# Performance work log

Hardware: AMD Instinct MI355X
Metric: run time of the kernel (lower is better)

The kernel has to match this reference:

```python
import jax, jax.numpy as jnp
import numpy as np

B, T, C, E = 16, 1024, 256, 512
NUM_CENTER = [512, 256, 128]
NUM_NNS = [16, 32, 64]
BN_EPS = 1e-5


def _fps(pts, K):
    # farthest point sampling, deterministic start at index 0. pts: [B,N,3] -> [B,K] int32
    N = pts.shape[1]
    def one(p):
        def step(carry, _):
            d, cur = carry
            dist = jnp.sum((p - p[cur]) ** 2, axis=-1)
            d = jnp.minimum(d, dist)
            nxt = jnp.argmax(d).astype(jnp.int32)
            return (d, nxt), cur
        init = (jnp.full((N,), jnp.inf, p.dtype), jnp.int32(0))
        _, idxs = jax.lax.scan(step, init, None, length=K)
        return idxs
    return jax.vmap(one)(pts)


def _knn(q, t, k):
    # k nearest neighbors of each query q [B,Tq,3] among targets t [B,Tt,3] -> [B,Tq,k]
    d2 = (jnp.sum(q * q, -1)[:, :, None] + jnp.sum(t * t, -1)[:, None, :]
          - 2.0 * jnp.einsum('bqc,btc->bqt', q, t))
    _, idx = jax.lax.top_k(-d2, k)
    return idx


def _gather(x, idx):
    # x [B,N,C], idx [B,M] -> [B,M,C]
    return jax.vmap(lambda xb, ib: xb[ib])(x, idx)


def _knn_gather(x, idx):
    # x [B,N,C], idx [B,M,K] -> [B,M,K,C]
    return jax.vmap(lambda xb, ib: xb[ib])(x, idx)


def _bn(x, g, b):
    # training-mode BatchNorm1d over leading (batch) dim of [N,C]
    m = jnp.mean(x, axis=0)
    v = jnp.mean((x - m) ** 2, axis=0)
    return (x - m) * jax.lax.rsqrt(v + BN_EPS) * g + b


def reference(tokens, centers, lrfs, wq, wkv, mlp_w1, mlp_b1, mlp_w2, mlp_b2,
              bn1_g, bn1_b, bn2_g, bn2_b, att_w1, att_b1, att_w2, att_b2,
              emb_w, emb_b, embn_g, embn_b):
    Bq, Tt, Cd = tokens.shape
    centers_target = centers
    lrfs_target = lrfs.reshape(Bq, Tt, 9)
    tokens_target = tokens
    T_target = Tt
    for i in range(len(NUM_CENTER)):
        Tq = NUM_CENTER[i]
        k = NUM_NNS[i]
        rep_idx = _fps(centers_target, Tq)                      # [B,Tq]
        centers_query = _gather(centers_target, rep_idx)        # [B,Tq,3]
        lrfs_query = _gather(lrfs_target, rep_idx)              # [B,Tq,9]
        tokens_query = _gather(tokens_target, rep_idx)          # [B,Tq,C]
        nn_idx = _knn(centers_query, centers_target, k)         # [B,Tq,k]
        skip = tokens_query.reshape(Bq * Tq, Cd)
        if i > 0:
            t = jnp.concatenate([tokens_query, tokens_target], axis=1)
            t = _bn(t.reshape(Bq * (Tq + T_target), Cd), bn1_g[i], bn1_b[i])
            t = t.reshape(Bq, Tq + T_target, Cd)
            tokens_query, tokens_target = t[:, :Tq, :], t[:, Tq:, :]
        Q = tokens_query @ wq[i]                                # [B,Tq,C]
        KV = tokens_target @ wkv[i]                             # [B,Tt,2C]
        Kf, Vf = KV[..., :Cd], KV[..., Cd:]
        Kn = _knn_gather(Kf, nn_idx).reshape(Bq * Tq, k, Cd)
        Vn = _knn_gather(Vf, nn_idx).reshape(Bq * Tq, k, Cd)
        Qf = Q.reshape(Bq * Tq, Cd)
        # vector self-attention: elementwise Q-K diff -> MLP -> softmax over neighbors
        diff = Qf[:, None, :] - Kn                              # [B*Tq,k,C]
        sim = jax.nn.relu(diff @ att_w1[i] + att_b1[i]) @ att_w2[i] + att_b2[i]
        A = jax.nn.softmax(sim, axis=1)
        tq = jnp.sum(A * Vn, axis=1)                            # [B*Tq,C]
        tq = tq + skip
        skip2 = tq
        tq = _bn(tq, bn2_g[i], bn2_b[i])
        tq = jax.nn.relu(tq @ mlp_w1[i] + mlp_b1[i]) @ mlp_w2[i] + mlp_b2[i]
        tq = tq + skip2
        T_target = Tq
        centers_target = centers_query
        lrfs_target = lrfs_query
        tokens_target = tq.reshape(Bq, Tq, Cd)
    g = jnp.mean(tokens_target, axis=1)                         # [B,C]
    g = jax.nn.relu(_bn(g @ emb_w + emb_b, embn_g, embn_b))     # [B,E]
    # ksparse: keep top-64 activations per row
    vals, _ = jax.lax.top_k(g, 64)
    thr = vals[:, -1:]
    g = jnp.where(g >= thr, g, 0.0)
    n = jnp.maximum(jnp.linalg.norm(g, axis=1, keepdims=True), 1e-12)
    return g / n


def setup_inputs() -> dict:
    key = jax.random.key(0)
    ks = jax.random.split(key, 10)
    s = 0.05
    return {
        'tokens': jax.random.normal(ks[0], (B, T, C), jnp.float32),
        'centers': jax.random.normal(ks[1], (B, T, 3), jnp.float32),
        'lrfs': jax.random.normal(ks[2], (B, T, 3, 3), jnp.float32),
        'wq': jax.random.normal(ks[3], (3, C, C), jnp.float32) * s,
        'wkv': jax.random.normal(ks[4], (3, C, 2 * C), jnp.float32) * s,
        'mlp_w1': jax.random.normal(ks[5], (3, C, 2 * C), jnp.float32) * s,
        'mlp_b1': jnp.zeros((3, 2 * C), jnp.float32),
        'mlp_w2': jax.random.normal(ks[6], (3, 2 * C, C), jnp.float32) * s,
        'mlp_b2': jnp.zeros((3, C), jnp.float32),
        'bn1_g': jnp.ones((3, C), jnp.float32),
        'bn1_b': jnp.zeros((3, C), jnp.float32),
        'bn2_g': jnp.ones((3, C), jnp.float32),
        'bn2_b': jnp.zeros((3, C), jnp.float32),
        'att_w1': jax.random.normal(ks[7], (3, C, C), jnp.float32) * s,
        'att_b1': jnp.zeros((3, C), jnp.float32),
        'att_w2': jax.random.normal(ks[8], (3, C, C), jnp.float32) * s,
        'att_b2': jnp.zeros((3, C), jnp.float32),
        'emb_w': jax.random.normal(ks[9], (C, E), jnp.float32) * s,
        'emb_b': jnp.zeros((E,), jnp.float32),
        'embn_g': jnp.ones((E,), jnp.float32),
        'embn_b': jnp.zeros((E,), jnp.float32),
    }
```

## Files before the change

### kernel.cpp

```cpp
#include <hip/hip_runtime.h>
#include <cstdint>
#include <cmath>

static constexpr int BB = 16;
static constexpr int TT0 = 1024;
static constexpr int CC = 256;
static constexpr int EE = 512;

typedef __bf16 bf16x8 __attribute__((ext_vector_type(8)));
typedef float  f32x4  __attribute__((ext_vector_type(4)));

template <int NPL>
__device__ void fps_body(float4* sp, const float* __restrict__ ctr,
                         int Tt, int Ksel, int* __restrict__ rep,
                         int b, int lane)
{
  const float* base = ctr + (size_t)b * Tt * 3;
  float x[NPL], y[NPL], z[NPL], d[NPL];
  #pragma unroll
  for (int j = 0; j < NPL; ++j) {
    int idx = lane * NPL + j;
    x[j] = base[idx * 3 + 0];
    y[j] = base[idx * 3 + 1];
    z[j] = base[idx * 3 + 2];
    d[j] = INFINITY;
    sp[idx] = make_float4(x[j], y[j], z[j], 0.f);
  }
  int cur = 0;
  for (int s = 0; s < Ksel; ++s) {
    if (lane == 0) rep[b * Ksel + s] = cur;
    float4 cpt = sp[cur];
    unsigned long long key = 0ull;
    #pragma unroll
    for (int j = 0; j < NPL; ++j) {
      float dx = __fsub_rn(x[j], cpt.x);
      float dy = __fsub_rn(y[j], cpt.y);
      float dz = __fsub_rn(z[j], cpt.z);
      float dist = __fadd_rn(__fadd_rn(__fmul_rn(dx, dx), __fmul_rn(dy, dy)),
                             __fmul_rn(dz, dz));
      float nd = fminf(d[j], dist);
      d[j] = nd;
      unsigned long long kj =
          ((unsigned long long)__float_as_uint(nd) << 32) |
          (unsigned)(0xFFFFFFFFu - (unsigned)(lane * NPL + j));
      key = (kj > key) ? kj : key;
    }
    float ld = __uint_as_float((unsigned)(key >> 32));
    float rm = ld;
    {
      int t;
      t = __builtin_amdgcn_mov_dpp(__float_as_int(rm), 0x121, 0xf, 0xf, false);
      rm = fmaxf(rm, __int_as_float(t));
      t = __builtin_amdgcn_mov_dpp(__float_as_int(rm), 0x122, 0xf, 0xf, false);
      rm = fmaxf(rm, __int_as_float(t));
      t = __builtin_amdgcn_mov_dpp(__float_as_int(rm), 0x124, 0xf, 0xf, false);
      rm = fmaxf(rm, __int_as_float(t));
      t = __builtin_amdgcn_mov_dpp(__float_as_int(rm), 0x128, 0xf, 0xf, false);
      rm = fmaxf(rm, __int_as_float(t));
    }
    float r0 = __uint_as_float((unsigned)__builtin_amdgcn_readlane(__float_as_int(rm), 0));
    float r1 = __uint_as_float((unsigned)__builtin_amdgcn_readlane(__float_as_int(rm), 16));
    float r2 = __uint_as_float((unsigned)__builtin_amdgcn_readlane(__float_as_int(rm), 32));
    float r3 = __uint_as_float((unsigned)__builtin_amdgcn_readlane(__float_as_int(rm), 48));
    float gm = fmaxf(fmaxf(r0, r1), fmaxf(r2, r3));
    unsigned long long mask = __ballot(ld == gm);
    int wl = __ffsll(mask) - 1;
    unsigned lowkey = (unsigned)__builtin_amdgcn_readlane((int)(unsigned)key, wl);
    cur = (int)(0xFFFFFFFFu - lowkey);
  }
}

__global__ __launch_bounds__(256) void knn_kernel(
    const float* __restrict__ cq, const float* __restrict__ ct,
    int Tq, int Tt, int Kn, int* __restrict__ nn)
{
  int r = blockIdx.x;
  int b = r / Tq;
  __shared__ float d2[1024];
  __shared__ float wv[4];
  __shared__ int wi[4];
  int tid = threadIdx.x, lane = tid & 63, wid = tid >> 6;
  float qx = cq[(size_t)r * 3 + 0];
  float qy = cq[(size_t)r * 3 + 1];
  float qz = cq[(size_t)r * 3 + 2];
  float sq = __fadd_rn(__fadd_rn(__fmul_rn(qx, qx), __fmul_rn(qy, qy)),
                       __fmul_rn(qz, qz));
  for (int t = tid; t < Tt; t += 256) {
    const float* tp = ct + ((size_t)b * Tt + t) * 3;
    float tx = tp[0], ty = tp[1], tz = tp[2];
    float st = __fadd_rn(__fadd_rn(__fmul_rn(tx, tx), __fmul_rn(ty, ty)),
                         __fmul_rn(tz, tz));
    float dot = __fadd_rn(__fadd_rn(__fmul_rn(qx, tx), __fmul_rn(qy, ty)),
                          __fmul_rn(qz, tz));
    d2[t] = __fsub_rn(__fadd_rn(sq, st), __fmul_rn(2.0f, dot));
  }
  __syncthreads();
  for (int j = 0; j < Kn; ++j) {
    float v = INFINITY; int ix = 0x7fffffff;
    for (int t = tid; t < Tt; t += 256) {
      float dv = d2[t];
      if (dv < v) { v = dv; ix = t; }
    }
    #pragma unroll
    for (int off = 32; off > 0; off >>= 1) {
      float ov = __shfl_down(v, off);
      int oi = __shfl_down(ix, off);
      if (ov < v || (ov == v && oi < ix)) { v = ov; ix = oi; }
    }
    if (lane == 0) { wv[wid] = v; wi[wid] = ix; }
    __syncthreads();
    if (tid == 0) {
      float bv = wv[0]; int bi = wi[0];
      for (int w = 1; w < 4; ++w)
        if (wv[w] < bv || (wv[w] == bv && wi[w] < bi)) { bv = wv[w]; bi = wi[w]; }
      nn[(size_t)r * Kn + j] = bi;
      d2[bi] = INFINITY;
    }
    __syncthreads();
  }
}

__global__ void gather_rows_kernel(
    const float* __restrict__ src, const int* __restrict__ idx,
    float* __restrict__ dst, int Tq, int Tt, int D, int total)
{
  int i = blockIdx.x * blockDim.x + threadIdx.x;
  if (i >= total) return;
  int d = i % D;
  int q = (i / D) % Tq;
  int b = i / (D * Tq);
  int s = idx[b * Tq + q];
  dst[i] = src[((size_t)b * Tt + s) * D + d];
}

__global__ __launch_bounds__(256) void bn_stats_kernel(
    const float* __restrict__ x1, int R1, const float* __restrict__ x2, int R2,
    float* __restrict__ part, int nch)
{
  int c = threadIdx.x;
  int chunk = blockIdx.x;
  int R = R1 + R2;
  int per = (R + nch - 1) / nch;
  int r0 = chunk * per;
  int r1 = min(r0 + per, R);
  float s = 0.f, ss = 0.f;
  for (int r = r0; r < r1; ++r) {
    float v = (r < R1) ? x1[(size_t)r * 256 + c] : x2[(size_t)(r - R1) * 256 + c];
    s += v;
    ss = fmaf(v, v, ss);
  }
  part[(size_t)chunk * 512 + c] = s;
  part[(size_t)chunk * 512 + 256 + c] = ss;
}

__global__ __launch_bounds__(256) void bn_finalize_kernel(
    const float* __restrict__ part, int nch, int R,
    float* __restrict__ mean, float* __restrict__ rstd)
{
  int c = threadIdx.x;
  float s = 0.f, ss = 0.f;
  for (int k = 0; k < nch; ++k) {
    s += part[(size_t)k * 512 + c];
    ss += part[(size_t)k * 512 + 256 + c];
  }
  float m = s / (float)R;
  float v = ss / (float)R - m * m;
  if (v < 0.f) v = 0.f;
  mean[c] = m;
  rstd[c] = rsqrtf(v + 1e-5f);
}

__global__ __launch_bounds__(256) void gemm_kernel(
    const float* __restrict__ A, int lda,
    const float* __restrict__ W, int ldw,
    const float* __restrict__ bias, const float* __restrict__ resid,
    float* __restrict__ out, int M, int N, int K, int relu)
{
  __shared__ float As[32][68];
  __shared__ float Bs[32][68];
  int bm = blockIdx.y * 64;
  int bn = blockIdx.x * 64;
  int tid = threadIdx.x;
  int tx = tid & 15, ty = tid >> 4;
  int arow = tid >> 3;
  int ak = (tid & 7) * 4;
  int wk = tid >> 4;
  int wn = (tid & 15) * 4;
  float acc[4][4] = {{0.f}};
  for (int k0 = 0; k0 < K; k0 += 32) {
    #pragma unroll
    for (int h = 0; h < 2; ++h) {
      int row = bm + arow + h * 32;
      float4 a = (row < M)
          ? *(const float4*)&A[(size_t)row * lda + k0 + ak]
          : make_float4(0.f, 0.f, 0.f, 0.f);
      As[ak + 0][arow + h * 32] = a.x;
      As[ak + 1][arow + h * 32] = a.y;
      As[ak + 2][arow + h * 32] = a.z;
      As[ak + 3][arow + h * 32] = a.w;
    }
    #pragma unroll
    for (int h = 0; h < 2; ++h) {
      int krow = k0 + wk + h * 16;
      *(float4*)&Bs[wk + h * 16][wn] =
          *(const float4*)&W[(size_t)krow * ldw + bn + wn];
    }
    __syncthreads();
    #pragma unroll
    for (int k = 0; k < 32; ++k) {
      float4 a = *(const float4*)&As[k][ty * 4];
      float4 b = *(const float4*)&Bs[k][tx * 4];
      float av[4] = {a.x, a.y, a.z, a.w};
      float bv[4] = {b.x, b.y, b.z, b.w};
      #pragma unroll
      for (int i = 0; i < 4; ++i)
        #pragma unroll
        for (int j = 0; j < 4; ++j)
          acc[i][j] = fmaf(av[i], bv[j], acc[i][j]);
    }
    __syncthreads();
  }
  #pragma unroll
  for (int i = 0; i < 4; ++i) {
    int m = bm + ty * 4 + i;
    if (m >= M) continue;
    #pragma unroll
    for (int j = 0; j < 4; ++j) {
      int n = bn + tx * 4 + j;
      float v = acc[i][j];
      if (bias) v += bias[n];
      if (relu) v = fmaxf(v, 0.f);
      if (resid) v += resid[(size_t)m * N + n];
      out[(size_t)m * N + n] = v;
    }
  }
}

__global__ void splitT_kernel(
    const float* __restrict__ src, int ldw, int K, int N,
    __bf16* __restrict__ hi, __bf16* __restrict__ lo, int total)
{
  int i = blockIdx.x * blockDim.x + threadIdx.x;
  if (i >= total) return;
  int n = i / K;
  int k = i - n * K;
  float v = src[(size_t)k * ldw + n];
  __bf16 h = (__bf16)v;
  hi[i] = h;
  lo[i] = (__bf16)(v - (float)h);
}

__global__ __launch_bounds__(256) void split_w2_kernel(
    const float* __restrict__ w2, __bf16* __restrict__ hi,
    __bf16* __restrict__ lo)
{
  int i = blockIdx.x * 256 + threadIdx.x;
  int s = i >> 16;
  int e = i & 65535;
  int cp = e >> 8;
  int cc = e & 255;
  float v = w2[((size_t)s << 16) + cc * 256 + cp];
  __bf16 h = (__bf16)v;
  hi[i] = h;
  lo[i] = (__bf16)(v - (float)h);
}

template <int NPL>
__global__ __launch_bounds__(256) void gemm_mfma_kernel(
    const float* __restrict__ A, int lda,
    const __bf16* __restrict__ WThi, const __bf16* __restrict__ WTlo,
    const float* __restrict__ bias, const float* __restrict__ resid,
    float* __restrict__ out, int M, int N, int K, int relu,
    const float* __restrict__ bnm, const float* __restrict__ bnr,
    const float* __restrict__ bng, const float* __restrict__ bnb,
    int nbx,
    const float* __restrict__ fps_ctr, int fps_Tt, int fps_Ksel,
    int* __restrict__ fps_rep)
{
  __shared__ __align__(16) float As[128 * 36];
  if ((int)blockIdx.x >= nbx) {
    if (fps_rep == nullptr || (int)blockIdx.y >= BB) return;
    if ((int)threadIdx.x >= 64) return;
    fps_body<NPL>((float4*)As, fps_ctr, fps_Tt, fps_Ksel, fps_rep,
                  blockIdx.y, threadIdx.x);
    return;
  }
  int bm = blockIdx.y * 128;
  int bn = blockIdx.x * 64;
  int tid = threadIdx.x;
  int w = tid >> 6, lane = tid & 63;
  int jl = lane & 15;
  int kg = lane >> 4;

  f32x4 acc[2][4];
  #pragma unroll
  for (int mt = 0; mt < 2; ++mt)
    #pragma unroll
    for (int nt = 0; nt < 4; ++nt) acc[mt][nt] = (f32x4){0.f, 0.f, 0.f, 0.f};

  for (int k0 = 0; k0 < K; k0 += 32) {
    #pragma unroll
    for (int f = 0; f < 4; ++f) {
      int fi = tid + f * 256;
      int row = fi >> 3, c4 = fi & 7;
      float4 v = *(const float4*)&A[(size_t)(bm + row) * lda + k0 + c4 * 4];
      if (bnm) {
        int kk = k0 + c4 * 4;
        float4 m4 = *(const float4*)&bnm[kk];
        float4 r4 = *(const float4*)&bnr[kk];
        float4 g4 = *(const float4*)&bng[kk];
        float4 b4 = *(const float4*)&bnb[kk];
        v.x = (v.x - m4.x) * r4.x * g4.x + b4.x;
        v.y = (v.y - m4.y) * r4.y * g4.y + b4.y;
        v.z = (v.z - m4.z) * r4.z * g4.z + b4.z;
        v.w = (v.w - m4.w) * r4.w * g4.w + b4.w;
      }
      *(float4*)&As[row * 36 + c4 * 4] = v;
    }
    __syncthreads();
    bf16x8 ahi[2], alo[2];
    #pragma unroll
    for (int mt = 0; mt < 2; ++mt) {
      int row = (w * 2 + mt) * 16 + jl;
      float4 a0 = *(const float4*)&As[row * 36 + kg * 8];
      float4 a1 = *(const float4*)&As[row * 36 + kg * 8 + 4];
      float hv[8] = {a0.x, a0.y, a0.z, a0.w, a1.x, a1.y, a1.z, a1.w};
      #pragma unroll
      for (int i = 0; i < 8; ++i) {
        __bf16 t0 = (__bf16)hv[i];
        ahi[mt][i] = t0;
        alo[mt][i] = (__bf16)(hv[i] - (float)t0);
      }
    }
    #pragma unroll
    for (int nt = 0; nt < 4; ++nt) {
      size_t boff = (size_t)(bn + nt * 16 + jl) * K + k0 + kg * 8;
      bf16x8 bhi = *(const bf16x8*)(WThi + boff);
      bf16x8 blo = *(const bf16x8*)(WTlo + boff);
      #pragma unroll
      for (int mt = 0; mt < 2; ++mt) {
        acc[mt][nt] = __builtin_amdgcn_mfma_f32_16x16x32_bf16(alo[mt], bhi, acc[mt][nt], 0, 0, 0);
        acc[mt][nt] = __builtin_amdgcn_mfma_f32_16x16x32_bf16(ahi[mt], blo, acc[mt][nt], 0, 0, 0);
        acc[mt][nt] = __builtin_amdgcn_mfma_f32_16x16x32_bf16(ahi[mt], bhi, acc[mt][nt], 0, 0, 0);
      }
    }
    __syncthreads();
  }
  #pragma unroll
  for (int mt = 0; mt < 2; ++mt)
    #pragma unroll
    for (int nt = 0; nt < 4; ++nt)
      #pragma unroll
      for (int qi = 0; qi < 4; ++qi) {
        int m = bm + (w * 2 + mt) * 16 + kg * 4 + qi;
        int n = bn + nt * 16 + jl;
        float v = acc[mt][nt][qi];
        if (bias) v += bias[n];
        if (relu) v = fmaxf(v, 0.f);
        if (resid) v += resid[(size_t)m * N + n];
        out[(size_t)m * N + n] = v;
      }
}

template <int KN>
__global__ __launch_bounds__(256, 2) void attn5_kernel(
    const float* __restrict__ Qw, const float* __restrict__ KV,
    const int* __restrict__ nn,
    const float* __restrict__ b1, const __bf16* __restrict__ w2Thi,
    const __bf16* __restrict__ w2Tlo, const float* __restrict__ b2,
    const float* __restrict__ skip, float* __restrict__ out, int Tq, int Tt)
{
  constexpr int G  = 128 / KN;
  constexpr int GC = 64 / KN;
  constexpr int LD = 260;
  __shared__ float sim[64 * LD];
  __shared__ int nns[128];
  int r0 = blockIdx.x * G;
  int b = r0 / Tq;
  int tid = threadIdx.x;
  if (tid < 128) nns[tid] = nn[(size_t)r0 * KN + tid];
  __syncthreads();

  int w = tid >> 6, lane = tid & 63;
  int jl = lane & 15;
  int kg = lane >> 4;
  int nt0 = w * 4;
  const float* kvb = KV + (size_t)b * Tt * 512;

  f32x4 acc[8][4];
  #pragma unroll
  for (int m = 0; m < 8; ++m)
    #pragma unroll
    for (int n = 0; n < 4; ++n) acc[m][n] = (f32x4){0.f, 0.f, 0.f, 0.f};

  const float* qp[8];
  const float* kp[8];
  #pragma unroll
  for (int mt = 0; mt < 8; ++mt) {
    int jr = mt * 16 + jl;
    qp[mt] = Qw + (size_t)(r0 + jr / KN) * 256;
    kp[mt] = kvb + (size_t)nns[jr] * 512;
  }

  #pragma unroll
  for (int ks = 0; ks < 8; ++ks) {
    int c0 = ks * 32 + kg * 8;
    float4 b1a = *(const float4*)(b1 + c0);
    float4 b1b = *(const float4*)(b1 + c0 + 4);
    bf16x8 ahi[8], alo[8];
    #pragma unroll
    for (int mt = 0; mt < 8; ++mt) {
      float4 qa = *(const float4*)(qp[mt] + c0);
      float4 qb = *(const float4*)(qp[mt] + c0 + 4);
      float4 ka = *(const float4*)(kp[mt] + c0);
      float4 kb = *(const float4*)(kp[mt] + c0 + 4);
      float h[8];
      h[0] = fmaxf(qa.x - ka.x + b1a.x, 0.f);
      h[1] = fmaxf(qa.y - ka.y + b1a.y, 0.f);
      h[2] = fmaxf(qa.z - ka.z + b1a.z, 0.f);
      h[3] = fmaxf(qa.w - ka.w + b1a.w, 0.f);
      h[4] = fmaxf(qb.x - kb.x + b1b.x, 0.f);
      h[5] = fmaxf(qb.y - kb.y + b1b.y, 0.f);
      h[6] = fmaxf(qb.z - kb.z + b1b.z, 0.f);
      h[7] = fmaxf(qb.w - kb.w + b1b.w, 0.f);
      #pragma unroll
      for (int i = 0; i < 8; ++i) {
        __bf16 t0 = (__bf16)h[i];
        ahi[mt][i] = t0;
        alo[mt][i] = (__bf16)(h[i] - (float)t0);
      }
    }
    #pragma unroll
    for (int t = 0; t < 4; ++t) {
      size_t boff = (size_t)((nt0 + t) * 16 + jl) * 256 + c0;
      bf16x8 bhi = *(const bf16x8*)(w2Thi + boff);
      bf16x8 blo = *(const bf16x8*)(w2Tlo + boff);
      #pragma unroll
      for (int mt = 0; mt < 8; ++mt) {
        acc[mt][t] = __builtin_amdgcn_mfma_f32_16x16x32_bf16(alo[mt], bhi, acc[mt][t], 0, 0, 0);
        acc[mt][t] = __builtin_amdgcn_mfma_f32_16x16x32_bf16(ahi[mt], blo, acc[mt][t], 0, 0, 0);
        acc[mt][t] = __builtin_amdgcn_mfma_f32_16x16x32_bf16(ahi[mt], bhi, acc[mt][t], 0, 0, 0);
      }
    }
  }

  int c = tid;
  float bb2 = b2[c];
  const float* vbb = kvb + 256;
  #pragma unroll
  for (int ch = 0; ch < 2; ++ch) {
    if (ch) __syncthreads();
    #pragma unroll
    for (int m2 = 0; m2 < 4; ++m2) {
      int mt = ch * 4 + m2;
      #pragma unroll
      for (int t = 0; t < 4; ++t)
        #pragma unroll
        for (int qi = 0; qi < 4; ++qi)
          sim[(m2 * 16 + kg * 4 + qi) * LD + (nt0 + t) * 16 + jl] = acc[mt][t][qi];
    }
    __syncthreads();
    #pragma unroll
    for (int gg = 0; gg < GC; ++gg) {
      int jb_l = gg * KN;
      int jb_g = ch * 64 + gg * KN;
      float m = -INFINITY;
      #pragma unroll 8
      for (int jj = 0; jj < KN; ++jj)
        m = fmaxf(m, sim[(jb_l + jj) * LD + c] + bb2);
      float ssum = 0.f, o = 0.f;
      #pragma unroll 8
      for (int jj = 0; jj < KN; ++jj) {
        float e = expf(sim[(jb_l + jj) * LD + c] + bb2 - m);
        ssum += e;
        o = fmaf(e, vbb[(size_t)nns[jb_g + jj] * 512 + c], o);
      }
      int r = r0 + ch * GC + gg;
      out[(size_t)r * 256 + c] = o / ssum + skip[(size_t)r * 256 + c];
    }
  }
}

__global__ void gmean_kernel(const float* __restrict__ tok,
                             float* __restrict__ out, int Tt)
{
  int i = blockIdx.x * blockDim.x + threadIdx.x;
  if (i >= BB * CC) return;
  int b = i >> 8;
  int c = i & 255;
  float s = 0.f;
  for (int t = 0; t < Tt; ++t) s += tok[((size_t)b * Tt + t) * 256 + c];
  out[i] = s / (float)Tt;
}

__global__ void embbn_kernel(const float* __restrict__ x,
                             const float* __restrict__ g,
                             const float* __restrict__ bta,
                             float* __restrict__ y)
{
  int e = blockIdx.x * blockDim.x + threadIdx.x;
  if (e >= EE) return;
  float s = 0.f;
  for (int r = 0; r < BB; ++r) s += x[r * EE + e];
  float m = s / (float)BB;
  float vs = 0.f;
  for (int r = 0; r < BB; ++r) {
    float d = x[r * EE + e] - m;
    vs = fmaf(d, d, vs);
  }
  float rs = rsqrtf(vs / (float)BB + 1e-5f);
  for (int r = 0; r < BB; ++r) {
    float val = (x[r * EE + e] - m) * rs * g[e] + bta[e];
    y[r * EE + e] = fmaxf(val, 0.f);
  }
}

__global__ __launch_bounds__(256) void topk_norm_kernel(
    const float* __restrict__ gin, float* __restrict__ out)
{
  int b = blockIdx.x, tid = threadIdx.x, lane = tid & 63, wid = tid >> 6;
  __shared__ float vals[512];
  __shared__ float wv[4];
  __shared__ int wi[4];
  __shared__ float sh;
  float g0 = gin[b * 512 + tid];
  float g1 = gin[b * 512 + 256 + tid];
  vals[tid] = g0;
  vals[256 + tid] = g1;
  __syncthreads();
  for (int it = 0; it < 64; ++it) {
    float v = vals[tid];
    int ix = tid;
    float u = vals[256 + tid];
    if (u > v) { v = u; ix = 256 + tid; }
    #pragma unroll
    for (int off = 32; off > 0; off >>= 1) {
      float ov = __shfl_down(v, off);
      int oi = __shfl_down(ix, off);
      if (ov > v || (ov == v && oi < ix)) { v = ov; ix = oi; }
    }
    if (lane == 0) { wv[wid] = v; wi[wid] = ix; }
    __syncthreads();
    if (tid == 0) {
      float bv = wv[0]; int bi = wi[0];
      for (int w = 1; w < 4; ++w)
        if (wv[w] > bv || (wv[w] == bv && wi[w] < bi)) { bv = wv[w]; bi = wi[w]; }
      vals[bi] = -INFINITY;
      sh = bv;
    }
    __syncthreads();
  }
  float thr = sh;
  float m0 = (g0 >= thr) ? g0 : 0.f;
  float m1 = (g1 >= thr) ? g1 : 0.f;
  float ss = m0 * m0 + m1 * m1;
  #pragma unroll
  for (int off = 32; off > 0; off >>= 1) ss += __shfl_down(ss, off);
  if (lane == 0) wv[wid] = ss;
  __syncthreads();
  if (tid == 0) {
    float t = wv[0] + wv[1] + wv[2] + wv[3];
    sh = fmaxf(sqrtf(t), 1e-12f);
  }
  __syncthreads();
  float n = sh;
  out[b * 512 + tid] = m0 / n;
  out[b * 512 + 256 + tid] = m1 / n;
}

extern "C" void kernel_launch(void* const* d_in, const int* in_sizes, int n_in,
                              void* d_out, int out_size, void* d_ws, size_t ws_size,
                              hipStream_t stream)
{
  const float* tokens  = (const float*)d_in[0];
  const float* centers = (const float*)d_in[1];
  const float* wq      = (const float*)d_in[3];
  const float* wkv     = (const float*)d_in[4];
  const float* mlp_w1  = (const float*)d_in[5];
  const float* mlp_b1  = (const float*)d_in[6];
  const float* mlp_w2  = (const float*)d_in[7];
  const float* mlp_b2  = (const float*)d_in[8];
  const float* bn1_g   = (const float*)d_in[9];
  const float* bn1_b   = (const float*)d_in[10];
  const float* bn2_g   = (const float*)d_in[11];
  const float* bn2_b   = (const float*)d_in[12];
  const float* att_w1  = (const float*)d_in[13];
  const float* att_b1  = (const float*)d_in[14];
  const float* att_w2  = (const float*)d_in[15];
  const float* att_b2  = (const float*)d_in[16];
  const float* emb_w   = (const float*)d_in[17];
  const float* emb_b   = (const float*)d_in[18];
  const float* embn_g  = (const float*)d_in[19];
  const float* embn_b  = (const float*)d_in[20];
  (void)in_sizes; (void)n_in; (void)out_size; (void)ws_size;

  char* ws = (char*)d_ws;
  size_t off = 0;
  auto alloc = [&](size_t bytes) -> void* {
    void* p = ws + off;
    off += (bytes + 255) & ~(size_t)255;
    return p;
  };
  const size_t tokMax  = (size_t)BB * 512 * CC * 4;
  float* tokA     = (float*)alloc(tokMax);
  float* tokB     = (float*)alloc(tokMax);
  float* ctrA     = (float*)alloc((size_t)BB * 512 * 3 * 4);
  float* ctrB     = (float*)alloc((size_t)BB * 256 * 3 * 4);
  float* ctrC     = (float*)alloc((size_t)BB * 128 * 3 * 4);
  float* tokq_raw = (float*)alloc(tokMax);
  float* Qw1      = (float*)alloc(tokMax);
  float* KVbuf    = (float*)alloc((size_t)BB * 1024 * 512 * 4);
  float* tq1      = (float*)alloc(tokMax);
  float* mlph     = (float*)alloc((size_t)BB * 512 * 512 * 4);
  float* WFq      = (float*)alloc((size_t)3 * CC * CC * 4);
  float* WFk      = (float*)alloc((size_t)3 * CC * CC * 4);
  __bf16* w2Thi   = (__bf16*)alloc((size_t)3 * CC * CC * 2);
  __bf16* w2Tlo   = (__bf16*)alloc((size_t)3 * CC * CC * 2);
  __bf16* wfqThi  = (__bf16*)alloc((size_t)3 * CC * CC * 2);
  __bf16* wfqTlo  = (__bf16*)alloc((size_t)3 * CC * CC * 2);
  __bf16* wkvThi  = (__bf16*)alloc((size_t)3 * 512 * CC * 2);
  __bf16* wkvTlo  = (__bf16*)alloc((size_t)3 * 512 * CC * 2);
  __bf16* w1Thi   = (__bf16*)alloc((size_t)3 * CC * 512 * 2);
  __bf16* w1Tlo   = (__bf16*)alloc((size_t)3 * CC * 512 * 2);
  __bf16* wm2Thi  = (__bf16*)alloc((size_t)3 * 512 * CC * 2);
  __bf16* wm2Tlo  = (__bf16*)alloc((size_t)3 * 512 * CC * 2);
  int*   rep0     = (int*)alloc((size_t)BB * 512 * 4);
  int*   rep1     = (int*)alloc((size_t)BB * 256 * 4);
  int*   rep2     = (int*)alloc((size_t)BB * 128 * 4);
  int*   nnb      = (int*)alloc((size_t)BB * 512 * 64 * 4);
  float* bnpart   = (float*)alloc((size_t)64 * 512 * 4);
  float* bn1mean  = (float*)alloc(256 * 4);
  float* bn1rstd  = (float*)alloc(256 * 4);
  float* bn2mean  = (float*)alloc(256 * 4);
  float* bn2rstd  = (float*)alloc(256 * 4);
  float* gmeanb   = (float*)alloc((size_t)BB * CC * 4);
  float* gembb    = (float*)alloc((size_t)BB * EE * 4);
  float* grelub   = (float*)alloc((size_t)BB * EE * 4);

  const int NC[3] = {512, 256, 128};
  const int NN[3] = {16, 32, 64};
  int* reps[3] = {rep0, rep1, rep2};
  float* ctrq[3] = {ctrA, ctrB, ctrC};

  for (int i = 0; i < 3; ++i) {
    gemm_kernel<<<dim3(4, 4), 256, 0, stream>>>(
        wq + (size_t)i * CC * CC, CC, att_w1 + (size_t)i * CC * CC, CC,
        nullptr, nullptr, WFq + (size_t)i * CC * CC, CC, CC, CC, 0);
    gemm_kernel<<<dim3(4, 4), 256, 0, stream>>>(
        wkv + (size_t)i * CC * 512, 512, att_w1 + (size_t)i * CC * CC, CC,
        nullptr, nullptr, WFk + (size_t)i * CC * CC, CC, CC, CC, 0);
  }
  split_w2_kernel<<<3 * 65536 / 256, 256, 0, stream>>>(att_w2, w2Thi, w2Tlo);
  for (int i = 0; i < 3; ++i) {
    int t1 = CC * CC;
    splitT_kernel<<<(t1 + 255) / 256, 256, 0, stream>>>(
        WFq + (size_t)i * CC * CC, CC, CC, CC,
        wfqThi + (size_t)i * t1, wfqTlo + (size_t)i * t1, t1);
    splitT_kernel<<<(t1 + 255) / 256, 256, 0, stream>>>(
        WFk + (size_t)i * CC * CC, CC, CC, CC,
        wkvThi + (size_t)i * 512 * CC, wkvTlo + (size_t)i * 512 * CC, t1);
    splitT_kernel<<<(t1 + 255) / 256, 256, 0, stream>>>(
        wkv + (size_t)i * CC * 512 + CC, 512, CC, CC,
        wkvThi + (size_t)i * 512 * CC + t1, wkvTlo + (size_t)i * 512 * CC + t1, t1);
    int t2 = CC * 512;
    splitT_kernel<<<(t2 + 255) / 256, 256, 0, stream>>>(
        mlp_w1 + (size_t)i * t2, 512, CC, 512,
        w1Thi + (size_t)i * t2, w1Tlo + (size_t)i * t2, t2);
    splitT_kernel<<<(t2 + 255) / 256, 256, 0, stream>>>(
        mlp_w2 + (size_t)i * t2, CC, 512, CC,
        wm2Thi + (size_t)i * t2, wm2Tlo + (size_t)i * t2, t2);
  }

  const float* cur_tok = tokens;
  const float* cur_ctr = centers;
  int curTt = TT0;
  float* tok_bufs[2] = {tokA, tokB};

  for (int i = 0; i < 3; ++i) {
    int Tq = NC[i], Kn = NN[i], Tt = curTt;
    float* ctr_q = ctrq[i];
    float* tok_next = tok_bufs[i & 1];
    int M = BB * Tq;
    int Mt = BB * Tt;
    int* rep = reps[i];

    const float *b1m = nullptr, *b1r = nullptr, *b1g = nullptr, *b1b = nullptr;

    if (i == 0) {
      gemm_mfma_kernel<16><<<dim3(512 / 64 + 1, Mt / 128), 256, 0, stream>>>(
          tokens, CC, wkvThi, wkvTlo, nullptr, nullptr, KVbuf,
          Mt, 512, CC, 0, nullptr, nullptr, nullptr, nullptr,
          512 / 64, centers, 1024, 512, rep0);
    }

    {
      int tot = BB * Tq * 3;
      gather_rows_kernel<<<(tot + 255) / 256, 256, 0, stream>>>(
          cur_ctr, rep, ctr_q, Tq, Tt, 3, tot);
    }
    {
      int tot = M * CC;
      gather_rows_kernel<<<(tot + 255) / 256, 256, 0, stream>>>(
          cur_tok, rep, tokq_raw, Tq, Tt, CC, tot);
    }
    knn_kernel<<<M, 256, 0, stream>>>(ctr_q, cur_ctr, Tq, Tt, Kn, nnb);

    if (i > 0) {
      bn_stats_kernel<<<64, 256, 0, stream>>>(tokq_raw, M, cur_tok, Mt, bnpart, 64);
      bn_finalize_kernel<<<1, 256, 0, stream>>>(bnpart, 64, M + Mt, bn1mean, bn1rstd);
      b1m = bn1mean; b1r = bn1rstd; b1g = bn1_g + i * CC; b1b = bn1_b + i * CC;
      if (i == 1)
        gemm_mfma_kernel<4><<<dim3(512 / 64 + 1, Mt / 128), 256, 0, stream>>>(
            cur_tok, CC, wkvThi + (size_t)i * 512 * CC, wkvTlo + (size_t)i * 512 * CC,
            nullptr, nullptr, KVbuf, Mt, 512, CC, 0, b1m, b1r, b1g, b1b,
            512 / 64, ctrB, 256, 128, rep2);
      else
        gemm_mfma_kernel<4><<<dim3(512 / 64, Mt / 128), 256, 0, stream>>>(
            cur_tok, CC, wkvThi + (size_t)i * 512 * CC, wkvTlo + (size_t)i * 512 * CC,
            nullptr, nullptr, KVbuf, Mt, 512, CC, 0, b1m, b1r, b1g, b1b,
            512 / 64, nullptr, 0, 0, nullptr);
    }

    gemm_mfma_kernel<4><<<dim3(CC / 64, M / 128), 256, 0, stream>>>(
        tokq_raw, CC, wfqThi + (size_t)i * CC * CC, wfqTlo + (size_t)i * CC * CC,
        nullptr, nullptr, Qw1, M, CC, CC, 0, b1m, b1r, b1g, b1b,
        CC / 64, nullptr, 0, 0, nullptr);

    if (Kn == 16)
      attn5_kernel<16><<<dim3(M / 8), 256, 0, stream>>>(
          Qw1, KVbuf, nnb, att_b1 + i * CC,
          w2Thi + (size_t)i * CC * CC, w2Tlo + (size_t)i * CC * CC,
          att_b2 + i * CC, tokq_raw, tq1, Tq, Tt);
    else if (Kn == 32)
      attn5_kernel<32><<<dim3(M / 4), 256, 0, stream>>>(
          Qw1, KVbuf, nnb, att_b1 + i * CC,
          w2Thi + (size_t)i * CC * CC, w2Tlo + (size_t)i * CC * CC,
          att_b2 + i * CC, tokq_raw, tq1, Tq, Tt);
    else
      attn5_kernel<64><<<dim3(M / 2), 256, 0, stream>>>(
          Qw1, KVbuf, nnb, att_b1 + i * CC,
          w2Thi + (size_t)i * CC * CC, w2Tlo + (size_t)i * CC * CC,
          att_b2 + i * CC, tokq_raw, tq1, Tq, Tt);

    bn_stats_kernel<<<64, 256, 0, stream>>>(tq1, M, tq1, 0, bnpart, 64);
    bn_finalize_kernel<<<1, 256, 0, stream>>>(bnpart, 64, M, bn2mean, bn2rstd);
    if (i == 0)
      gemm_mfma_kernel<8><<<dim3(512 / 64 + 1, M / 128), 256, 0, stream>>>(
          tq1, CC, w1Thi + (size_t)i * CC * 512, w1Tlo + (size_t)i * CC * 512,
          mlp_b1 + i * 512, nullptr, mlph, M, 512, CC, 1,
          bn2mean, bn2rstd, bn2_g + i * CC, bn2_b + i * CC,
          512 / 64, ctrA, 512, 256, rep1);
    else
      gemm_mfma_kernel<4><<<dim3(512 / 64, M / 128), 256, 0, stream>>>(
          tq1, CC, w1Thi + (size_t)i * CC * 512, w1Tlo + (size_t)i * CC * 512,
          mlp_b1 + i * 512, nullptr, mlph, M, 512, CC, 1,
          bn2mean, bn2rstd, bn2_g + i * CC, bn2_b + i * CC,
          512 / 64, nullptr, 0, 0, nullptr);
    gemm_mfma_kernel<4><<<dim3(CC / 64, M / 128), 256, 0, stream>>>(
        mlph, 512, wm2Thi + (size_t)i * 512 * CC, wm2Tlo + (size_t)i * 512 * CC,
        mlp_b2 + i * CC, tq1, tok_next, M, CC, 512, 0,
        nullptr, nullptr, nullptr, nullptr,
        CC / 64, nullptr, 0, 0, nullptr);

    cur_tok = tok_next;
    cur_ctr = ctr_q;
    curTt = Tq;
  }

  gmean_kernel<<<(BB * CC + 255) / 256, 256, 0, stream>>>(cur_tok, gmeanb, curTt);
  gemm_kernel<<<dim3(EE / 64, 1), 256, 0, stream>>>(
      gmeanb, CC, emb_w, EE, emb_b, nullptr, gembb, BB, EE, CC, 0);
  embbn_kernel<<<2, 256, 0, stream>>>(gembb, embn_g, embn_b, grelub);
  topk_norm_kernel<<<BB, 256, 0, stream>>>(grelub, (float*)d_out);
}
```

Before: 1.834 ms.

## Run kNN selection per wavefront with register-resident packed distance keys

Replaces the block-per-query kNN, which kept distances in shared memory and ran two block barriers per selected neighbor, with a wave-per-query kernel. Each lane keeps its share of candidates as 64-bit keys (order-preserving distance bits plus index) in registers. Each selection step uses a DPP/readlane wave reduction with no barriers. Ties resolve toward the lower index, as before. The cost is more registers per lane, which grow with the target count, and an assumption that Tt equals 64 times the per-lane count.

New measurement: 1.605 ms. 1.14x faster.

```diff
diff --git a/kernel.cpp b/kernel.cpp
--- a/kernel.cpp
+++ b/kernel.cpp
@@ -70,53 +70,65 @@
   }
 }
 
-__global__ __launch_bounds__(256) void knn_kernel(
+template <int NPL2>
+__global__ __launch_bounds__(256) void knn_wave_kernel(
     const float* __restrict__ cq, const float* __restrict__ ct,
     int Tq, int Tt, int Kn, int* __restrict__ nn)
 {
-  int r = blockIdx.x;
+  int wid = threadIdx.x >> 6, lane = threadIdx.x & 63;
+  int r = blockIdx.x * 4 + wid;
   int b = r / Tq;
-  __shared__ float d2[1024];
-  __shared__ float wv[4];
-  __shared__ int wi[4];
-  int tid = threadIdx.x, lane = tid & 63, wid = tid >> 6;
+  const float* tb = ct + (size_t)b * Tt * 3;
   float qx = cq[(size_t)r * 3 + 0];
   float qy = cq[(size_t)r * 3 + 1];
   float qz = cq[(size_t)r * 3 + 2];
   float sq = __fadd_rn(__fadd_rn(__fmul_rn(qx, qx), __fmul_rn(qy, qy)),
                        __fmul_rn(qz, qz));
-  for (int t = tid; t < Tt; t += 256) {
-    const float* tp = ct + ((size_t)b * Tt + t) * 3;
-    float tx = tp[0], ty = tp[1], tz = tp[2];
+  unsigned long long key[NPL2];
+  #pragma unroll
+  for (int j = 0; j < NPL2; ++j) {
+    int t = lane * NPL2 + j;
+    float tx = tb[t * 3 + 0], ty = tb[t * 3 + 1], tz = tb[t * 3 + 2];
     float st = __fadd_rn(__fadd_rn(__fmul_rn(tx, tx), __fmul_rn(ty, ty)),
                          __fmul_rn(tz, tz));
     float dot = __fadd_rn(__fadd_rn(__fmul_rn(qx, tx), __fmul_rn(qy, ty)),
                           __fmul_rn(qz, tz));
-    d2[t] = __fsub_rn(__fadd_rn(sq, st), __fmul_rn(2.0f, dot));
-  }
-  __syncthreads();
-  for (int j = 0; j < Kn; ++j) {
-    float v = INFINITY; int ix = 0x7fffffff;
-    for (int t = tid; t < Tt; t += 256) {
-      float dv = d2[t];
-      if (dv < v) { v = dv; ix = t; }
-    }
-    #pragma unroll
-    for (int off = 32; off > 0; off >>= 1) {
-      float ov = __shfl_down(v, off);
-      int oi = __shfl_down(ix, off);
-      if (ov < v || (ov == v && oi < ix)) { v = ov; ix = oi; }
-    }
-    if (lane == 0) { wv[wid] = v; wi[wid] = ix; }
-    __syncthreads();
-    if (tid == 0) {
-      float bv = wv[0]; int bi = wi[0];
-      for (int w = 1; w < 4; ++w)
-        if (wv[w] < bv || (wv[w] == bv && wi[w] < bi)) { bv = wv[w]; bi = wi[w]; }
-      nn[(size_t)r * Kn + j] = bi;
-      d2[bi] = INFINITY;
-    }
-    __syncthreads();
+    float d2 = __fsub_rn(__fadd_rn(sq, st), __fmul_rn(2.0f, dot));
+    unsigned ub = __float_as_uint(d2);
+    ub ^= (ub >> 31) ? 0xFFFFFFFFu : 0x80000000u;
+    key[j] = ((unsigned long long)ub << 32) | (unsigned)t;
+  }
+  for (int k = 0; k < Kn; ++k) {
+    unsigned long long lmin = ~0ull;
+    #pragma unroll
+    for (int j = 0; j < NPL2; ++j) lmin = (key[j] < lmin) ? key[j] : lmin;
+    unsigned md = (unsigned)(lmin >> 32);
+    unsigned rm = md;
+    {
+      unsigned t;
+      t = (unsigned)__builtin_amdgcn_mov_dpp((int)rm, 0x121, 0xf, 0xf, false);
+      rm = (t < rm) ? t : rm;
+      t = (unsigned)__builtin_amdgcn_mov_dpp((int)rm, 0x122, 0xf, 0xf, false);
+      rm = (t < rm) ? t : rm;
+      t = (unsigned)__builtin_amdgcn_mov_dpp((int)rm, 0x124, 0xf, 0xf, false);
+      rm = (t < rm) ? t : rm;
+      t = (unsigned)__builtin_amdgcn_mov_dpp((int)rm, 0x128, 0xf, 0xf, false);
+      rm = (t < rm) ? t : rm;
+    }
+    unsigned r0 = (unsigned)__builtin_amdgcn_readlane((int)rm, 0);
+    unsigned r1 = (unsigned)__builtin_amdgcn_readlane((int)rm, 16);
+    unsigned r2 = (unsigned)__builtin_amdgcn_readlane((int)rm, 32);
+    unsigned r3 = (unsigned)__builtin_amdgcn_readlane((int)rm, 48);
+    unsigned g01 = (r0 < r1) ? r0 : r1;
+    unsigned g23 = (r2 < r3) ? r2 : r3;
+    unsigned gmin = (g01 < g23) ? g01 : g23;
+    unsigned long long mask = __ballot(md == gmin);
+    int wl = __ffsll(mask) - 1;
+    int wt = __builtin_amdgcn_readlane((int)(unsigned)lmin, wl);
+    if (lane == 0) nn[(size_t)r * Kn + k] = wt;
+    #pragma unroll
+    for (int j = 0; j < NPL2; ++j)
+      if (lane * NPL2 + j == wt) key[j] = ~0ull;
   }
 }
 
@@ -703,7 +715,12 @@
       gather_rows_kernel<<<(tot + 255) / 256, 256, 0, stream>>>(
           cur_tok, rep, tokq_raw, Tq, Tt, CC, tot);
     }
-    knn_kernel<<<M, 256, 0, stream>>>(ctr_q, cur_ctr, Tq, Tt, Kn, nnb);
+    if (Tt == 1024)
+      knn_wave_kernel<16><<<M / 4, 256, 0, stream>>>(ctr_q, cur_ctr, Tq, Tt, Kn, nnb);
+    else if (Tt == 512)
+      knn_wave_kernel<8><<<M / 4, 256, 0, stream>>>(ctr_q, cur_ctr, Tq, Tt, Kn, nnb);
+    else
+      knn_wave_kernel<4><<<M / 4, 256, 0, stream>>>(ctr_q, cur_ctr, Tq, Tt, Kn, nnb);
 
     if (i > 0) {
       bn_stats_kernel<<<64, 256, 0, stream>>>(tokq_raw, M, cur_tok, Mt, bnpart, 64);
```
